# Performance work log

Hardware: AMD Instinct MI355X
Metric: run time of the kernel (lower is better)

## Reference

```python
import jax, jax.numpy as jnp
import numpy as np


def setup_inputs() -> dict:
    key = jax.random.key(0)
    k1, k2 = jax.random.split(key)
    N, CIN, VDIM = 16384, 2048, 128  # v_dim = max(cin//16, 10)
    x = jax.random.normal(k1, (N, CIN), dtype=jnp.float32)
    Fq = jax.random.normal(k2, (CIN, VDIM), dtype=jnp.float32)
    Fq = Fq / jnp.linalg.norm(Fq, axis=0, keepdims=True)  # init normalizes columns
    by = jnp.zeros((CIN,), dtype=jnp.float32)
    return {"x": x, "Fq": Fq, "by": by}


def reference(x, Fq, by):
    # Sequential Householder reflections: x <- x - 2 (x v) v^T for each column v of Fq.
    def step(x, v):
        v = v / jnp.linalg.norm(v)          # [cin]
        proj = x @ v                         # [N]
        x = x - 2.0 * proj[:, None] * v[None, :]
        return x, None

    x, _ = jax.lax.scan(step, x, Fq.T)       # scan over v_dim columns
    return x + by
```

## Files before the change

### kernel.cpp

```cpp
#include <hip/hip_runtime.h>

#define NR   16384
#define CIN  2048
#define VDIM 128
#define SPLITK 4
#define KSL  (CIN / SPLITK)

#define FMA4(accv, s, bv) { accv.x += (s)*(bv).x; accv.y += (s)*(bv).y; accv.z += (s)*(bv).z; accv.w += (s)*(bv).w; }

__global__ __launch_bounds__(256) void k_normalize(const float* __restrict__ Fq,
                                                   float* __restrict__ V,
                                                   float* __restrict__ Vt) {
    int k = blockIdx.x;
    __shared__ float red[256];
    float ss = 0.f;
    for (int i = threadIdx.x; i < CIN; i += 256) {
        float v = Fq[i * VDIM + k];
        ss += v * v;
    }
    red[threadIdx.x] = ss;
    __syncthreads();
    for (int off = 128; off > 0; off >>= 1) {
        if (threadIdx.x < off) red[threadIdx.x] += red[threadIdx.x + off];
        __syncthreads();
    }
    float inv = 1.0f / sqrtf(red[0]);
    for (int i = threadIdx.x; i < CIN; i += 256) {
        float v = Fq[i * VDIM + k] * inv;
        V[i * VDIM + k] = v;
        Vt[k * CIN + i] = v;
    }
}

__global__ __launch_bounds__(64) void k_gram(const float* __restrict__ Vt,
                                             float* __restrict__ G) {
    int j = blockIdx.x, k = blockIdx.y;
    int lane = threadIdx.x;
    const float* a = Vt + j * CIN;
    const float* b = Vt + k * CIN;
    float s = 0.f;
    for (int i = lane * 4; i < CIN; i += 64 * 4) {
        float4 av = *(const float4*)(a + i);
        float4 bv = *(const float4*)(b + i);
        s += av.x * bv.x + av.y * bv.y + av.z * bv.z + av.w * bv.w;
    }
    #pragma unroll
    for (int off = 32; off > 0; off >>= 1) s += __shfl_down(s, off, 64);
    if (lane == 0) G[j * VDIM + k] = s;
}

__global__ __launch_bounds__(256) void k_P(const float* __restrict__ X,
                                           const float* __restrict__ V,
                                           float* __restrict__ Pp) {
    __shared__ float xs[2][16][132];
    __shared__ float vs[2][16][132];
    int tid = threadIdx.x;
    int rowbase = blockIdx.x * 128;
    int kstart = blockIdx.y * KSL;
    float* P = Pp + (size_t)blockIdx.y * NR * VDIM;

    int r0 = (tid >> 4) << 2;
    int c0 = (tid & 15) << 2;
    int arow = tid >> 1;
    int aq   = (tid & 1) << 3;
    int brow = tid >> 5;
    int bcol = (tid & 31) << 2;

    float4 acc[2][2][4];
    #pragma unroll
    for (int a = 0; a < 2; ++a)
        #pragma unroll
        for (int b = 0; b < 2; ++b)
            #pragma unroll
            for (int i = 0; i < 4; ++i) acc[a][b][i] = make_float4(0.f, 0.f, 0.f, 0.f);

    const float* xsrc = X + (size_t)(rowbase + arow) * CIN + kstart + aq;

    float4 avA, avB, bvA, bvB;
    avA = *(const float4*)(xsrc);
    avB = *(const float4*)(xsrc + 4);
    {
        const float4* vp = (const float4*)(V + (size_t)kstart * VDIM);
        bvA = vp[tid]; bvB = vp[tid + 256];
    }
    xs[0][aq + 0][arow] = avA.x; xs[0][aq + 1][arow] = avA.y;
    xs[0][aq + 2][arow] = avA.z; xs[0][aq + 3][arow] = avA.w;
    xs[0][aq + 4][arow] = avB.x; xs[0][aq + 5][arow] = avB.y;
    xs[0][aq + 6][arow] = avB.z; xs[0][aq + 7][arow] = avB.w;
    *(float4*)&vs[0][brow][bcol]     = bvA;
    *(float4*)&vs[0][brow + 8][bcol] = bvB;
    __syncthreads();

    const int NT = KSL / 16;
    for (int t = 0; t < NT; ++t) {
        int cur = t & 1;
        if (t + 1 < NT) {
            const float* xp = xsrc + (t + 1) * 16;
            avA = *(const float4*)(xp);
            avB = *(const float4*)(xp + 4);
            const float4* vp = (const float4*)(V + (size_t)(kstart + (t + 1) * 16) * VDIM);
            bvA = vp[tid]; bvB = vp[tid + 256];
        }
        #pragma unroll
        for (int kk = 0; kk < 16; ++kk) {
            float4 a0 = *(const float4*)&xs[cur][kk][r0];
            float4 a1 = *(const float4*)&xs[cur][kk][r0 + 64];
            float4 b0 = *(const float4*)&vs[cur][kk][c0];
            float4 b1 = *(const float4*)&vs[cur][kk][c0 + 64];
            float ar0[4] = {a0.x, a0.y, a0.z, a0.w};
            float ar1[4] = {a1.x, a1.y, a1.z, a1.w};
            #pragma unroll
            for (int i = 0; i < 4; ++i) {
                FMA4(acc[0][0][i], ar0[i], b0);
                FMA4(acc[0][1][i], ar0[i], b1);
                FMA4(acc[1][0][i], ar1[i], b0);
                FMA4(acc[1][1][i], ar1[i], b1);
            }
        }
        if (t + 1 == NT) break;
        int nxt = cur ^ 1;
        xs[nxt][aq + 0][arow] = avA.x; xs[nxt][aq + 1][arow] = avA.y;
        xs[nxt][aq + 2][arow] = avA.z; xs[nxt][aq + 3][arow] = avA.w;
        xs[nxt][aq + 4][arow] = avB.x; xs[nxt][aq + 5][arow] = avB.y;
        xs[nxt][aq + 6][arow] = avB.z; xs[nxt][aq + 7][arow] = avB.w;
        *(float4*)&vs[nxt][brow][bcol]     = bvA;
        *(float4*)&vs[nxt][brow + 8][bcol] = bvB;
        __syncthreads();
    }

    #pragma unroll
    for (int qr = 0; qr < 2; ++qr)
        #pragma unroll
        for (int i = 0; i < 4; ++i) {
            size_t row = rowbase + qr * 64 + r0 + i;
            *(float4*)(P + row * VDIM + c0)      = acc[qr][0][i];
            *(float4*)(P + row * VDIM + c0 + 64) = acc[qr][1][i];
        }
}

__global__ __launch_bounds__(256) void k_solve(const float* __restrict__ Pp,
                                               const float* __restrict__ G,
                                               float* __restrict__ S) {
    int lane = threadIdx.x & 63;
    int wv = threadIdx.x >> 6;
    int row0 = (blockIdx.x * 4 + wv) * 4;

    float p0[4], p1[4], s0[4], s1[4];
    #pragma unroll
    for (int r = 0; r < 4; ++r) {
        size_t base = (size_t)(row0 + r) * VDIM;
        float a0 = 0.f, a1 = 0.f;
        #pragma unroll
        for (int y = 0; y < SPLITK; ++y) {
            a0 += Pp[(size_t)y * NR * VDIM + base + lane];
            a1 += Pp[(size_t)y * NR * VDIM + base + 64 + lane];
        }
        p0[r] = a0; p1[r] = a1;
        s0[r] = 0.f; s1[r] = 0.f;
    }
    float gj0 = G[lane], gj1 = G[64 + lane];
    for (int j = 0; j < VDIM; ++j) {
        float g0 = gj0, g1 = gj1;
        if (j + 1 < VDIM) {
            gj0 = G[(j + 1) * VDIM + lane];
            gj1 = G[(j + 1) * VDIM + 64 + lane];
        }
        float c[4];
        #pragma unroll
        for (int r = 0; r < 4; ++r) {
            float t0 = (lane < j)      ? s0[r] * g0 : 0.f;
            float t1 = (64 + lane < j) ? s1[r] * g1 : 0.f;
            c[r] = t0 + t1;
        }
        #pragma unroll
        for (int off = 1; off < 64; off <<= 1) {
            #pragma unroll
            for (int r = 0; r < 4; ++r) c[r] += __shfl_xor(c[r], off, 64);
        }
        if (j < 64) {
            if (lane == j) {
                #pragma unroll
                for (int r = 0; r < 4; ++r) s0[r] = 2.f * (p0[r] - c[r]);
            }
        } else {
            if (lane == j - 64) {
                #pragma unroll
                for (int r = 0; r < 4; ++r) s1[r] = 2.f * (p1[r] - c[r]);
            }
        }
    }
    #pragma unroll
    for (int r = 0; r < 4; ++r) {
        S[(size_t)(row0 + r) * VDIM + lane]      = s0[r];
        S[(size_t)(row0 + r) * VDIM + 64 + lane] = s1[r];
    }
}

__global__ __launch_bounds__(256) void k_out(const float* __restrict__ X,
                                             const float* __restrict__ S,
                                             const float* __restrict__ Vt,
                                             const float* __restrict__ by,
                                             float* __restrict__ out) {
    __shared__ float st[2][16][132];
    __shared__ float vt[2][16][132];
    int tid = threadIdx.x;
    int rb = blockIdx.y * 128;
    int cb = blockIdx.x * 128;
    int r0 = (tid >> 4) << 2;
    int c0 = (tid & 15) << 2;

    int srow = tid >> 1;
    int sq   = (tid & 1) << 3;
    int vk   = tid >> 4;
    int vm   = (tid & 15) << 3;

    float4 acc[2][2][4];
    #pragma unroll
    for (int a = 0; a < 2; ++a)
        #pragma unroll
        for (int b = 0; b < 2; ++b)
            #pragma unroll
            for (int i = 0; i < 4; ++i) acc[a][b][i] = make_float4(0.f, 0.f, 0.f, 0.f);

    const float* ssrc  = S  + (size_t)(rb + srow) * VDIM + sq;
    const float* vtsrc = Vt + (size_t)vk * CIN + cb + vm;

    float4 sA, sB, vA, vB;
    sA = *(const float4*)(ssrc);
    sB = *(const float4*)(ssrc + 4);
    vA = *(const float4*)(vtsrc);
    vB = *(const float4*)(vtsrc + 4);
    st[0][sq + 0][srow] = sA.x; st[0][sq + 1][srow] = sA.y;
    st[0][sq + 2][srow] = sA.z; st[0][sq + 3][srow] = sA.w;
    st[0][sq + 4][srow] = sB.x; st[0][sq + 5][srow] = sB.y;
    st[0][sq + 6][srow] = sB.z; st[0][sq + 7][srow] = sB.w;
    *(float4*)&vt[0][vk][vm]     = vA;
    *(float4*)&vt[0][vk][vm + 4] = vB;
    __syncthreads();

    const int NT = VDIM / 16;
    for (int t = 0; t < NT; ++t) {
        int cur = t & 1;
        if (t + 1 < NT) {
            const float* sp = ssrc + (t + 1) * 16;
            sA = *(const float4*)(sp);
            sB = *(const float4*)(sp + 4);
            const float* vp = vtsrc + (size_t)(t + 1) * 16 * CIN;
            vA = *(const float4*)(vp);
            vB = *(const float4*)(vp + 4);
        }
        #pragma unroll
        for (int kk = 0; kk < 16; ++kk) {
            float4 a0 = *(const float4*)&st[cur][kk][r0];
            float4 a1 = *(const float4*)&st[cur][kk][r0 + 64];
            float4 b0 = *(const float4*)&vt[cur][kk][c0];
            float4 b1 = *(const float4*)&vt[cur][kk][c0 + 64];
            float ar0[4] = {a0.x, a0.y, a0.z, a0.w};
            float ar1[4] = {a1.x, a1.y, a1.z, a1.w};
            #pragma unroll
            for (int i = 0; i < 4; ++i) {
                FMA4(acc[0][0][i], ar0[i], b0);
                FMA4(acc[0][1][i], ar0[i], b1);
                FMA4(acc[1][0][i], ar1[i], b0);
                FMA4(acc[1][1][i], ar1[i], b1);
            }
        }
        if (t + 1 == NT) break;
        int nxt = cur ^ 1;
        st[nxt][sq + 0][srow] = sA.x; st[nxt][sq + 1][srow] = sA.y;
        st[nxt][sq + 2][srow] = sA.z; st[nxt][sq + 3][srow] = sA.w;
        st[nxt][sq + 4][srow] = sB.x; st[nxt][sq + 5][srow] = sB.y;
        st[nxt][sq + 6][srow] = sB.z; st[nxt][sq + 7][srow] = sB.w;
        *(float4*)&vt[nxt][vk][vm]     = vA;
        *(float4*)&vt[nxt][vk][vm + 4] = vB;
        __syncthreads();
    }

    float4 by0 = *(const float4*)(by + cb + c0);
    float4 by1 = *(const float4*)(by + cb + c0 + 64);
    #pragma unroll
    for (int qr = 0; qr < 2; ++qr)
        #pragma unroll
        for (int i = 0; i < 4; ++i) {
            size_t row = rb + qr * 64 + r0 + i;
            float4 xv0 = *(const float4*)(X + row * CIN + cb + c0);
            float4 xv1 = *(const float4*)(X + row * CIN + cb + c0 + 64);
            float4 o0, o1;
            o0.x = xv0.x - acc[qr][0][i].x + by0.x;
            o0.y = xv0.y - acc[qr][0][i].y + by0.y;
            o0.z = xv0.z - acc[qr][0][i].z + by0.z;
            o0.w = xv0.w - acc[qr][0][i].w + by0.w;
            o1.x = xv1.x - acc[qr][1][i].x + by1.x;
            o1.y = xv1.y - acc[qr][1][i].y + by1.y;
            o1.z = xv1.z - acc[qr][1][i].z + by1.z;
            o1.w = xv1.w - acc[qr][1][i].w + by1.w;
            *(float4*)(out + row * CIN + cb + c0)      = o0;
            *(float4*)(out + row * CIN + cb + c0 + 64) = o1;
        }
}

extern "C" void kernel_launch(void* const* d_in, const int* in_sizes, int n_in,
                              void* d_out, int out_size, void* d_ws, size_t ws_size,
                              hipStream_t stream) {
    const float* x  = (const float*)d_in[0];
    const float* Fq = (const float*)d_in[1];
    const float* by = (const float*)d_in[2];
    float* out = (float*)d_out;
    float* ws = (float*)d_ws;

    float* V  = ws;
    float* Vt = ws + 262144;
    float* G  = ws + 524288;
    float* S  = ws + 540672;
    float* Pp = out;

    k_normalize<<<VDIM, 256, 0, stream>>>(Fq, V, Vt);
    k_gram<<<dim3(VDIM, VDIM), 64, 0, stream>>>(Vt, G);
    k_P<<<dim3(NR / 128, SPLITK), 256, 0, stream>>>(x, V, Pp);
    k_solve<<<NR / 16, 256, 0, stream>>>(Pp, G, S);
    k_out<<<dim3(CIN / 128, NR / 128), 256, 0, stream>>>(x, S, Vt, by, out);
}
```

Baseline: 559.0 us.

## Move triangular Householder solve from per-row to per-column weight matrix

Replaces the per-row sequential triangular solve (k_solve, 16384 rows x 128 serial steps with wave shuffles) with a back-substitution applied once to the reflector matrix, producing a modified weight matrix W (128 x 2048). The output then becomes x - P W + by, where P is the plain projection. This needs only a simple split-K reduction kernel over rows. The serial dependency chain now runs over 2048 columns in 16 small blocks instead of all rows, which may be latency-bound but handles far less total work.

New measurement: 667.8 us. +19.5%, slower.

```diff
diff --git a/kernel.cpp b/kernel.cpp
--- a/kernel.cpp
+++ b/kernel.cpp
@@ -47,6 +47,33 @@
     #pragma unroll
     for (int off = 32; off > 0; off >>= 1) s += __shfl_down(s, off, 64);
     if (lane == 0) G[j * VDIM + k] = s;
+}
+
+__global__ __launch_bounds__(128) void k_W(const float* __restrict__ Vt,
+                                           const float* __restrict__ G,
+                                           float* __restrict__ W) {
+    __shared__ float w[VDIM][128];
+    int c = threadIdx.x;
+    int cb = blockIdx.x * 128;
+    #pragma unroll 4
+    for (int k = 0; k < VDIM; ++k)
+        w[k][c] = 2.f * Vt[(size_t)k * CIN + cb + c];
+    for (int i = VDIM - 2; i >= 0; --i) {
+        const float* gi = G + i * VDIM;
+        float a0 = 0.f, a1 = 0.f, a2 = 0.f, a3 = 0.f;
+        int k = i + 1;
+        for (; k + 3 < VDIM; k += 4) {
+            a0 += gi[k + 0] * w[k + 0][c];
+            a1 += gi[k + 1] * w[k + 1][c];
+            a2 += gi[k + 2] * w[k + 2][c];
+            a3 += gi[k + 3] * w[k + 3][c];
+        }
+        for (; k < VDIM; ++k) a0 += gi[k] * w[k][c];
+        w[i][c] -= 2.f * ((a0 + a1) + (a2 + a3));
+    }
+    #pragma unroll 4
+    for (int k = 0; k < VDIM; ++k)
+        W[(size_t)k * CIN + cb + c] = w[k][c];
 }
 
 __global__ __launch_bounds__(256) void k_P(const float* __restrict__ X,
@@ -138,67 +165,24 @@
         }
 }
 
-__global__ __launch_bounds__(256) void k_solve(const float* __restrict__ Pp,
-                                               const float* __restrict__ G,
-                                               float* __restrict__ S) {
-    int lane = threadIdx.x & 63;
-    int wv = threadIdx.x >> 6;
-    int row0 = (blockIdx.x * 4 + wv) * 4;
-
-    float p0[4], p1[4], s0[4], s1[4];
-    #pragma unroll
-    for (int r = 0; r < 4; ++r) {
-        size_t base = (size_t)(row0 + r) * VDIM;
-        float a0 = 0.f, a1 = 0.f;
-        #pragma unroll
-        for (int y = 0; y < SPLITK; ++y) {
-            a0 += Pp[(size_t)y * NR * VDIM + base + lane];
-            a1 += Pp[(size_t)y * NR * VDIM + base + 64 + lane];
-        }
-        p0[r] = a0; p1[r] = a1;
-        s0[r] = 0.f; s1[r] = 0.f;
-    }
-    float gj0 = G[lane], gj1 = G[64 + lane];
-    for (int j = 0; j < VDIM; ++j) {
-        float g0 = gj0, g1 = gj1;
-        if (j + 1 < VDIM) {
-            gj0 = G[(j + 1) * VDIM + lane];
-            gj1 = G[(j + 1) * VDIM + 64 + lane];
-        }
-        float c[4];
-        #pragma unroll
-        for (int r = 0; r < 4; ++r) {
-            float t0 = (lane < j)      ? s0[r] * g0 : 0.f;
-            float t1 = (64 + lane < j) ? s1[r] * g1 : 0.f;
-            c[r] = t0 + t1;
-        }
-        #pragma unroll
-        for (int off = 1; off < 64; off <<= 1) {
-            #pragma unroll
-            for (int r = 0; r < 4; ++r) c[r] += __shfl_xor(c[r], off, 64);
-        }
-        if (j < 64) {
-            if (lane == j) {
-                #pragma unroll
-                for (int r = 0; r < 4; ++r) s0[r] = 2.f * (p0[r] - c[r]);
-            }
-        } else {
-            if (lane == j - 64) {
-                #pragma unroll
-                for (int r = 0; r < 4; ++r) s1[r] = 2.f * (p1[r] - c[r]);
-            }
-        }
-    }
-    #pragma unroll
-    for (int r = 0; r < 4; ++r) {
-        S[(size_t)(row0 + r) * VDIM + lane]      = s0[r];
-        S[(size_t)(row0 + r) * VDIM + 64 + lane] = s1[r];
-    }
+__global__ __launch_bounds__(256) void k_reduce(const float* __restrict__ Pp,
+                                                float* __restrict__ P) {
+    size_t idx = ((size_t)blockIdx.x * 256 + threadIdx.x) * 4;
+    float4 a = *(const float4*)(Pp + idx);
+    float4 b = *(const float4*)(Pp + (size_t)NR * VDIM + idx);
+    float4 c = *(const float4*)(Pp + (size_t)2 * NR * VDIM + idx);
+    float4 d = *(const float4*)(Pp + (size_t)3 * NR * VDIM + idx);
+    float4 o;
+    o.x = (a.x + b.x) + (c.x + d.x);
+    o.y = (a.y + b.y) + (c.y + d.y);
+    o.z = (a.z + b.z) + (c.z + d.z);
+    o.w = (a.w + b.w) + (c.w + d.w);
+    *(float4*)(P + idx) = o;
 }
 
 __global__ __launch_bounds__(256) void k_out(const float* __restrict__ X,
-                                             const float* __restrict__ S,
-                                             const float* __restrict__ Vt,
+                                             const float* __restrict__ P,
+                                             const float* __restrict__ W,
                                              const float* __restrict__ by,
                                              float* __restrict__ out) {
     __shared__ float st[2][16][132];
@@ -222,8 +206,8 @@
             #pragma unroll
             for (int i = 0; i < 4; ++i) acc[a][b][i] = make_float4(0.f, 0.f, 0.f, 0.f);
 
-    const float* ssrc  = S  + (size_t)(rb + srow) * VDIM + sq;
-    const float* vtsrc = Vt + (size_t)vk * CIN + cb + vm;
+    const float* ssrc  = P + (size_t)(rb + srow) * VDIM + sq;
+    const float* vtsrc = W + (size_t)vk * CIN + cb + vm;
 
     float4 sA, sB, vA, vB;
     sA = *(const float4*)(ssrc);
@@ -311,12 +295,14 @@
     float* V  = ws;
     float* Vt = ws + 262144;
     float* G  = ws + 524288;
-    float* S  = ws + 540672;
+    float* W  = ws + 540672;
+    float* P  = ws + 802816;
     float* Pp = out;
 
     k_normalize<<<VDIM, 256, 0, stream>>>(Fq, V, Vt);
     k_gram<<<dim3(VDIM, VDIM), 64, 0, stream>>>(Vt, G);
     k_P<<<dim3(NR / 128, SPLITK), 256, 0, stream>>>(x, V, Pp);
-    k_solve<<<NR / 16, 256, 0, stream>>>(Pp, G, S);
-    k_out<<<dim3(CIN / 128, NR / 128), 256, 0, stream>>>(x, S, Vt, by, out);
-}
+    k_W<<<CIN / 128, 128, 0, stream>>>(Vt, G, W);
+    k_reduce<<<(NR * VDIM) / 1024, 256, 0, stream>>>(Pp, P);
+    k_out<<<dim3(CIN / 128, NR / 128), 256, 0, stream>>>(x, P, W, by, out);
+}
```
